# Performance work log

Hardware: AMD Instinct MI355X
Metric: run time of the kernel (lower is better)

## Reference

```python
import jax, jax.numpy as jnp
import numpy as np


def _conv(x, w, padding):
    # x: NCHW, w: OIHW
    return jax.lax.conv_general_dilated(
        x, w, window_strides=(1, 1), padding=padding,
        dimension_numbers=('NCHW', 'OIHW', 'NCHW'))


def setup_inputs() -> dict:
    key = jax.random.key(0)
    ks = jax.random.split(key, 4)
    B, Cin, H, W = 128, 1024, 14, 14
    planes, expansion = 256, 4
    x = jax.random.normal(ks[0], (B, Cin, H, W), dtype=jnp.float32)
    # conv weights (layouts are fully dense since rho=0.0)
    w1 = jax.random.normal(ks[1], (planes, Cin, 1, 1), dtype=jnp.float32) * 0.02
    w2 = jax.random.normal(ks[2], (planes, planes, 3, 3), dtype=jnp.float32) * 0.02
    w3 = jax.random.normal(ks[3], (planes * expansion, planes, 1, 1), dtype=jnp.float32) * 0.02
    # Fixup scalar biases / scale
    z = jnp.zeros((1,), dtype=jnp.float32)
    return {
        'x': x, 'w1': w1, 'w2': w2, 'w3': w3,
        'bias1b': z, 'bias2a': z, 'bias2b': z, 'bias3a': z, 'bias3b': z,
        'rscale': jnp.ones((1,), dtype=jnp.float32), 'rbias': z,
    }


def reference(x, w1, w2, w3, bias1b, bias2a, bias2b, bias3a, bias3b, rscale, rbias):
    # conv1(x) + bias1b  (1x1, fused output bias)
    out = _conv(x, w1, 'VALID') + bias1b[0]
    # conv2(out + bias2a) + bias2b  (3x3, pad 1, fused input+output bias)
    out = _conv(out + bias2a[0], w2, 'SAME') + bias2b[0]
    # conv3(out + bias3a) + bias3b  (1x1)
    out = _conv(out + bias3a[0], w3, 'VALID') + bias3b[0]
    # fused scale + bias + residual ReLU: relu(out*rscale + rbias + identity)
    return jax.nn.relu(out * rscale[0] + rbias[0] + x)
```

## Files before the change

### kernel.cpp

```cpp
#include <hip/hip_runtime.h>
#include <stdint.h>

typedef __bf16 bf16x8 __attribute__((ext_vector_type(8)));
typedef float f32x4 __attribute__((ext_vector_type(4)));
typedef unsigned short u16;

__device__ __forceinline__ u16 f2bf(float f){
  uint32_t u = __float_as_uint(f);
  u = (u + 0x7fffu + ((u >> 16) & 1u)) >> 16;
  return (u16)u;
}
__device__ __forceinline__ float bf2f(u16 v){
  return __uint_as_float(((uint32_t)v) << 16);
}
__device__ __forceinline__ void gl_lds16(const void* g, void* l){
  __builtin_amdgcn_global_load_lds((const __attribute__((address_space(1))) void*)g,
                                   (__attribute__((address_space(3))) void*)l, 16, 0, 0);
}

__global__ __launch_bounds__(256) void prep_w(
    const float* __restrict__ w1, const float* __restrict__ w2,
    const float* __restrict__ w3, u16* __restrict__ wb1, u16* __restrict__ wb2,
    u16* __restrict__ wb3){
  int bid = blockIdx.x, t = threadIdx.x;
  if (bid < 1024){
    int i = bid*256 + t; wb1[i] = f2bf(w1[i]);
  } else if (bid < 3328){
    int i = (bid-1024)*256 + t;
    int o = i / 2304, r = i - o*2304, kq = r >> 8, c = r & 255;
    wb2[i] = f2bf(w2[((size_t)o*256 + c)*9 + kq]);
  } else {
    int i = (bid-3328)*256 + t; wb3[i] = f2bf(w3[i]);
  }
}

__global__ __launch_bounds__(256) void transform_x(const float* __restrict__ x,
                                                   u16* __restrict__ xp0){
  __shared__ float lds[64*201];
  const int b = blockIdx.y, c0 = blockIdx.x*64, t = threadIdx.x;
  const float4* src = (const float4*)x + (size_t)b*50176 + (size_t)c0*49;
  #pragma unroll
  for (int r = 0; r < 13; ++r){
    int q = r*256 + t;
    if (q < 3136){
      unsigned c = (unsigned)q / 49u, f = (unsigned)q - c*49u;
      float4 v = src[q];
      float* d = &lds[c*201 + f*4];
      d[0]=v.x; d[1]=v.y; d[2]=v.z; d[3]=v.w;
    }
  }
  __syncthreads();
  const int c4 = (t & 15)*4, pg = t >> 4;
  #pragma unroll
  for (int r = 0; r < 13; ++r){
    int p = r*16 + pg;
    if (p < 196){
      ushort4 pk;
      ((u16*)&pk)[0] = f2bf(lds[(c4+0)*201 + p]);
      ((u16*)&pk)[1] = f2bf(lds[(c4+1)*201 + p]);
      ((u16*)&pk)[2] = f2bf(lds[(c4+2)*201 + p]);
      ((u16*)&pk)[3] = f2bf(lds[(c4+3)*201 + p]);
      *(ushort4*)&xp0[((size_t)b*196 + p)*1024 + c0 + c4] = pk;
    }
  }
}

__global__ __launch_bounds__(512, 1) void gemm1_conv(
    const u16* __restrict__ A, const u16* __restrict__ B, u16* __restrict__ O,
    const float* __restrict__ s0, const float* __restrict__ s1){
  extern __shared__ char lds[];
  const int t = threadIdx.x, lane = t & 63, w = t >> 6;
  const int wm = (w >> 2) * 64, wn = (w & 3) * 64;
  const int b = blockIdx.x & 127, m0 = (blockIdx.x >> 7) * 128;
  f32x4 acc[4][4] = {};

  uint32_t aoff[2], boff[4];
  #pragma unroll
  for (int i = 0; i < 2; ++i){
    int gl = i*512 + t, row = gl >> 3, ss = gl & 7;
    aoff[i] = (uint32_t)(m0 + row)*2048 + ((ss ^ (row & 7)) << 4);
  }
  #pragma unroll
  for (int i = 0; i < 4; ++i){
    int gl = i*512 + t, row = gl >> 3, ss = gl & 7;
    int y = row >> 4, x = row & 15;
    int p = ((unsigned)(y-1) < 14u && (unsigned)(x-1) < 14u) ? (y-1)*14 + (x-1) : 0;
    boff[i] = ((uint32_t)b*196 + p)*2048 + ((ss ^ (row & 7)) << 4);
  }

  auto stage = [&](int buf, int kc){
    char* Ab = lds + buf*16384;
    char* Bb = lds + 32768 + buf*32768;
    #pragma unroll
    for (int i = 0; i < 2; ++i)
      gl_lds16((const char*)A + aoff[i] + kc*128, Ab + (i*512 + t)*16);
    #pragma unroll
    for (int i = 0; i < 4; ++i)
      gl_lds16((const char*)B + boff[i] + kc*128, Bb + (i*512 + t)*16);
  };
  auto compute = [&](int buf){
    char* Ab = lds + buf*16384;
    char* Bb = lds + 32768 + buf*32768;
    #pragma unroll
    for (int h = 0; h < 2; ++h){
      bf16x8 af[4], bfr[4];
      #pragma unroll
      for (int i = 0; i < 4; ++i){
        int row = wm + i*16 + (lane & 15);
        af[i] = *(const bf16x8*)(Ab + row*128 + (((h*4 + (lane>>4)) ^ (row & 7)) << 4));
      }
      #pragma unroll
      for (int j = 0; j < 4; ++j){
        int row = wn + j*16 + (lane & 15);
        bfr[j] = *(const bf16x8*)(Bb + row*128 + (((h*4 + (lane>>4)) ^ (row & 7)) << 4));
      }
      #pragma unroll
      for (int i = 0; i < 4; ++i)
        #pragma unroll
        for (int j = 0; j < 4; ++j)
          acc[i][j] = __builtin_amdgcn_mfma_f32_16x16x32_bf16(af[i], bfr[j], acc[i][j], 0, 0, 0);
    }
  };

  stage(0, 0);
  __syncthreads();
  #pragma unroll
  for (int kc = 0; kc < 16; ++kc){
    if (kc < 15) stage((kc+1) & 1, kc+1);
    compute(kc & 1);
    __syncthreads();
  }

  float badd = s0[0] + s1[0];
  #pragma unroll
  for (int i = 0; i < 4; ++i){
    int o = m0 + wm + i*16 + ((lane >> 4) << 2);
    #pragma unroll
    for (int j = 0; j < 4; ++j){
      int n = wn + j*16 + (lane & 15);
      int y = n >> 4, x = n & 15;
      bool real = ((unsigned)(y-1) < 14u) && ((unsigned)(x-1) < 14u);
      ushort4 pk;
      #pragma unroll
      for (int q = 0; q < 4; ++q)
        ((u16*)&pk)[q] = real ? f2bf(acc[i][j][q] + badd) : (u16)0;
      *(ushort4*)(O + ((size_t)b*256 + n)*256 + o) = pk;
    }
  }
}

__global__ __launch_bounds__(512, 1) void gemm2_conv(
    const u16* __restrict__ A, const u16* __restrict__ B, u16* __restrict__ O,
    const float* __restrict__ s0, const float* __restrict__ s1){
  extern __shared__ char lds[];
  const int t = threadIdx.x, lane = t & 63, w = t >> 6;
  const int wm = (w >> 2) * 64, wn = (w & 3) * 64;
  const int b = blockIdx.x & 127, m0 = (blockIdx.x >> 7) * 128;
  f32x4 acc[4][4] = {};

  uint32_t aoff[2], boff[5];
  #pragma unroll
  for (int i = 0; i < 2; ++i){
    int gl = i*512 + t, row = gl >> 3, ss = gl & 7;
    aoff[i] = (uint32_t)(m0 + row)*4608 + ((ss ^ (row & 7)) << 4);
  }
  #pragma unroll
  for (int i = 0; i < 5; ++i){
    int gl = i*512 + t, row = gl >> 3, ss = gl & 7;
    int pos = row - 18;
    pos = pos < 0 ? 0 : (pos > 255 ? 255 : pos);
    boff[i] = ((uint32_t)b*256 + pos)*512 + ((ss ^ (row & 7)) << 4);
  }

  auto stageA = [&](int buf, int kq, int kc){
    char* Ab = lds + buf*16384;
    int off = kq*512 + kc*128;
    #pragma unroll
    for (int i = 0; i < 2; ++i)
      gl_lds16((const char*)A + aoff[i] + off, Ab + (i*512 + t)*16);
  };
  auto stageB = [&](int buf, int kc){
    char* Bb = lds + 32768 + buf*37376;
    #pragma unroll
    for (int i = 0; i < 5; ++i){
      int gl = i*512 + t;
      if (gl < 2336) gl_lds16((const char*)B + boff[i] + kc*128, Bb + gl*16);
    }
  };
  auto compute = [&](int ab, int bb, int shift){
    char* Ab = lds + ab*16384;
    char* Bb = lds + 32768 + bb*37376;
    #pragma unroll
    for (int h = 0; h < 2; ++h){
      bf16x8 af[4], bfr[4];
      #pragma unroll
      for (int i = 0; i < 4; ++i){
        int row = wm + i*16 + (lane & 15);
        af[i] = *(const bf16x8*)(Ab + row*128 + (((h*4 + (lane>>4)) ^ (row & 7)) << 4));
      }
      #pragma unroll
      for (int j = 0; j < 4; ++j){
        int row = 18 + wn + j*16 + (lane & 15) + shift;
        bfr[j] = *(const bf16x8*)(Bb + row*128 + (((h*4 + (lane>>4)) ^ (row & 7)) << 4));
      }
      #pragma unroll
      for (int i = 0; i < 4; ++i)
        #pragma unroll
        for (int j = 0; j < 4; ++j)
          acc[i][j] = __builtin_amdgcn_mfma_f32_16x16x32_bf16(af[i], bfr[j], acc[i][j], 0, 0, 0);
    }
  };

  stageB(0, 0); stageA(0, 0, 0);
  __syncthreads();
  int ab = 0, bbuf = 0;
  #pragma unroll
  for (int kc = 0; kc < 4; ++kc){
    #pragma unroll
    for (int kq = 0; kq < 9; ++kq){
      if (kq < 8) stageA(ab ^ 1, kq + 1, kc);
      else if (kc < 3){ stageB(bbuf ^ 1, kc + 1); stageA(ab ^ 1, 0, kc + 1); }
      compute(ab, bbuf, (kq/3 - 1)*16 + (kq%3) - 1);
      __syncthreads();
      ab ^= 1;
      if (kq == 8) bbuf ^= 1;
    }
  }

  float badd = s0[0] + s1[0];
  #pragma unroll
  for (int i = 0; i < 4; ++i){
    int o = m0 + wm + i*16 + ((lane >> 4) << 2);
    #pragma unroll
    for (int j = 0; j < 4; ++j){
      int n = wn + j*16 + (lane & 15);
      int y = n >> 4, x = n & 15;
      if (((unsigned)(y-1) < 14u) && ((unsigned)(x-1) < 14u)){
        int p = (y-1)*14 + (x-1);
        ushort4 pk;
        #pragma unroll
        for (int q = 0; q < 4; ++q) ((u16*)&pk)[q] = f2bf(acc[i][j][q] + badd);
        *(ushort4*)(O + ((size_t)b*196 + p)*256 + o) = pk;
      }
    }
  }
}

__global__ __launch_bounds__(256, 4) void gemm3_conv(
    const u16* __restrict__ A, const u16* __restrict__ B, const u16* __restrict__ xresb,
    float* __restrict__ Of32, const float* __restrict__ s0, const float* __restrict__ s1,
    const float* __restrict__ s2){
  __shared__ char lds[33792];
  const int t = threadIdx.x, lane = t & 63, w = t >> 6;
  const int wm = (w >> 1) * 64, wn = (w & 1) * 64;
  const int orig = blockIdx.x;
  const int bid  = (orig & 7) * ((int)gridDim.x >> 3) + (orig >> 3);
  const int n0 = (bid >> 3) * 128, m0 = (bid & 7) * 128;
  f32x4 acc[4][4] = {};

  uint32_t aoff[4], boff[4];
  #pragma unroll
  for (int i = 0; i < 4; ++i){
    int gl = i*256 + t, row = gl >> 3, ss = gl & 7;
    int xo = (ss ^ (row & 7)) << 4;
    aoff[i] = (uint32_t)(m0 + row)*512 + xo;
    boff[i] = (uint32_t)(n0 + row)*512 + xo;
  }

  auto stage = [&](int s){
    char* Ab = lds;
    char* Bb = lds + 16384;
    #pragma unroll
    for (int i = 0; i < 4; ++i){
      gl_lds16((const char*)A + aoff[i] + s*128, Ab + (i*256 + t)*16);
      gl_lds16((const char*)B + boff[i] + s*128, Bb + (i*256 + t)*16);
    }
  };
  auto compute = [&](){
    char* Ab = lds;
    char* Bb = lds + 16384;
    #pragma unroll
    for (int h = 0; h < 2; ++h){
      bf16x8 af[4], bfr[4];
      #pragma unroll
      for (int i = 0; i < 4; ++i){
        int row = wm + i*16 + (lane & 15);
        af[i] = *(const bf16x8*)(Ab + row*128 + (((h*4 + (lane>>4)) ^ (row & 7)) << 4));
      }
      #pragma unroll
      for (int j = 0; j < 4; ++j){
        int row = wn + j*16 + (lane & 15);
        bfr[j] = *(const bf16x8*)(Bb + row*128 + (((h*4 + (lane>>4)) ^ (row & 7)) << 4));
      }
      #pragma unroll
      for (int i = 0; i < 4; ++i)
        #pragma unroll
        for (int j = 0; j < 4; ++j)
          acc[i][j] = __builtin_amdgcn_mfma_f32_16x16x32_bf16(af[i], bfr[j], acc[i][j], 0, 0, 0);
    }
  };

  #pragma unroll
  for (int s = 0; s < 4; ++s){
    if (s) __syncthreads();
    stage(s);
    __syncthreads();
    compute();
  }

  float b3 = s0[0], rs = s1[0], rbv = s2[0];
  float* ldsF = (float*)lds;
  #pragma unroll
  for (int pass = 0; pass < 2; ++pass){
    __syncthreads();
    if ((wm >> 6) == pass){
      #pragma unroll
      for (int i = 0; i < 4; ++i){
        int rb = i*16 + ((lane >> 4) << 2);
        #pragma unroll
        for (int j = 0; j < 4; ++j){
          int col = wn + j*16 + (lane & 15);
          #pragma unroll
          for (int q = 0; q < 4; ++q) ldsF[(rb + q)*132 + col] = acc[i][j][q];
        }
      }
    }
    __syncthreads();
    #pragma unroll
    for (int r = 0; r < 8; ++r){
      int row = (w << 4) + ((lane >> 5) << 3) + r;
      int n4  = (lane & 31) << 2;
      float4 v = *(float4*)&ldsF[row*132 + n4];
      uint32_t n = n0 + n4;
      uint32_t b = n / 196u, p = n - b*196u;
      int o = m0 + pass*64 + row;
      size_t base = ((size_t)b*1024 + o)*196 + p;
      const u16* xr = xresb + (size_t)n*1024 + o;
      float4 ov;
      ov.x = fmaxf((v.x + b3)*rs + rbv + bf2f(xr[0]),    0.f);
      ov.y = fmaxf((v.y + b3)*rs + rbv + bf2f(xr[1024]), 0.f);
      ov.z = fmaxf((v.z + b3)*rs + rbv + bf2f(xr[2048]), 0.f);
      ov.w = fmaxf((v.w + b3)*rs + rbv + bf2f(xr[3072]), 0.f);
      *(float4*)&Of32[base] = ov;
    }
  }
}

extern "C" void kernel_launch(void* const* d_in, const int* in_sizes, int n_in,
                              void* d_out, int out_size, void* d_ws, size_t ws_size,
                              hipStream_t stream){
  (void)in_sizes; (void)n_in; (void)out_size; (void)ws_size;
  const float* x   = (const float*)d_in[0];
  const float* w1  = (const float*)d_in[1];
  const float* w2  = (const float*)d_in[2];
  const float* w3  = (const float*)d_in[3];
  const float* b1b = (const float*)d_in[4];
  const float* b2a = (const float*)d_in[5];
  const float* b2b = (const float*)d_in[6];
  const float* b3a = (const float*)d_in[7];
  const float* b3b = (const float*)d_in[8];
  const float* rsc = (const float*)d_in[9];
  const float* rbi = (const float*)d_in[10];

  char* ws  = (char*)d_ws;
  u16*  xp1 = (u16*)ws;
  u16*  xp2 = (u16*)(ws + 16777216);
  u16*  xp0 = (u16*)(ws + 29622272);
  u16*  wb1 = (u16*)(ws + 81002496);
  u16*  wb2 = (u16*)(ws + 81526784);
  u16*  wb3 = (u16*)(ws + 82706432);

  prep_w     <<<dim3(4352),   256, 0, stream>>>(w1, w2, w3, wb1, wb2, wb3);
  transform_x<<<dim3(16,128), 256, 0, stream>>>(x, xp0);

  gemm1_conv<<<dim3(256),  512,  98304, stream>>>(wb1, xp0, xp1, b1b, b2a);
  gemm2_conv<<<dim3(256),  512, 107520, stream>>>(wb2, xp1, xp2, b2b, b3a);
  gemm3_conv<<<dim3(1568), 256,      0, stream>>>(wb3, xp2, xp0, (float*)d_out, b3b, rsc, rbi);
}
```

Before: 320.0 us.

## Merge prep kernels, shrink GEMM LDS footprints, read fp32 residual directly

Weight conversion and the x transpose now run in one launch, which removes a kernel launch. gemm1 moves to a smaller K-step with 4-way swizzle and 48KB static LDS, and gemm2 single-buffers the B halo tile to cut LDS from 105KB to 70KB. Both are meant to allow more resident blocks, although 512-thread blocks with 4-per-CU bounds may pressure registers. Block-to-batch mapping changes so the two M halves of a batch are adjacent. The epilogue reads the fp32 residual x directly and coalesced instead of strided bf16, which also fixes a precision loss on the residual. The cost is stalls on gemm2's B reloads, which are no longer overlapped.

```diff
diff --git a/kernel.cpp b/kernel.cpp
--- a/kernel.cpp
+++ b/kernel.cpp
@@ -10,18 +10,17 @@
   u = (u + 0x7fffu + ((u >> 16) & 1u)) >> 16;
   return (u16)u;
 }
-__device__ __forceinline__ float bf2f(u16 v){
-  return __uint_as_float(((uint32_t)v) << 16);
-}
 __device__ __forceinline__ void gl_lds16(const void* g, void* l){
   __builtin_amdgcn_global_load_lds((const __attribute__((address_space(1))) void*)g,
                                    (__attribute__((address_space(3))) void*)l, 16, 0, 0);
 }
 
-__global__ __launch_bounds__(256) void prep_w(
+__global__ __launch_bounds__(256) void prep_transform(
     const float* __restrict__ w1, const float* __restrict__ w2,
-    const float* __restrict__ w3, u16* __restrict__ wb1, u16* __restrict__ wb2,
-    u16* __restrict__ wb3){
+    const float* __restrict__ w3, const float* __restrict__ x,
+    u16* __restrict__ wb1, u16* __restrict__ wb2, u16* __restrict__ wb3,
+    u16* __restrict__ xp0){
+  __shared__ float lds[64*201];
   int bid = blockIdx.x, t = threadIdx.x;
   if (bid < 1024){
     int i = bid*256 + t; wb1[i] = f2bf(w1[i]);
@@ -29,133 +28,121 @@
     int i = (bid-1024)*256 + t;
     int o = i / 2304, r = i - o*2304, kq = r >> 8, c = r & 255;
     wb2[i] = f2bf(w2[((size_t)o*256 + c)*9 + kq]);
+  } else if (bid < 4352){
+    int i = (bid-3328)*256 + t; wb3[i] = f2bf(w3[i]);
   } else {
-    int i = (bid-3328)*256 + t; wb3[i] = f2bf(w3[i]);
-  }
-}
-
-__global__ __launch_bounds__(256) void transform_x(const float* __restrict__ x,
-                                                   u16* __restrict__ xp0){
-  __shared__ float lds[64*201];
-  const int b = blockIdx.y, c0 = blockIdx.x*64, t = threadIdx.x;
-  const float4* src = (const float4*)x + (size_t)b*50176 + (size_t)c0*49;
-  #pragma unroll
-  for (int r = 0; r < 13; ++r){
-    int q = r*256 + t;
-    if (q < 3136){
-      unsigned c = (unsigned)q / 49u, f = (unsigned)q - c*49u;
-      float4 v = src[q];
-      float* d = &lds[c*201 + f*4];
-      d[0]=v.x; d[1]=v.y; d[2]=v.z; d[3]=v.w;
-    }
-  }
+    int lin = bid - 4352;
+    int b = lin >> 4, c0 = (lin & 15)*64;
+    const float4* src = (const float4*)x + (size_t)b*50176 + (size_t)c0*49;
+    #pragma unroll
+    for (int r = 0; r < 13; ++r){
+      int q = r*256 + t;
+      if (q < 3136){
+        unsigned c = (unsigned)q / 49u, f = (unsigned)q - c*49u;
+        float4 v = src[q];
+        float* d = &lds[c*201 + f*4];
+        d[0]=v.x; d[1]=v.y; d[2]=v.z; d[3]=v.w;
+      }
+    }
+    __syncthreads();
+    const int c4 = (t & 15)*4, pg = t >> 4;
+    #pragma unroll
+    for (int r = 0; r < 13; ++r){
+      int p = r*16 + pg;
+      if (p < 196){
+        ushort4 pk;
+        ((u16*)&pk)[0] = f2bf(lds[(c4+0)*201 + p]);
+        ((u16*)&pk)[1] = f2bf(lds[(c4+1)*201 + p]);
+        ((u16*)&pk)[2] = f2bf(lds[(c4+2)*201 + p]);
+        ((u16*)&pk)[3] = f2bf(lds[(c4+3)*201 + p]);
+        *(ushort4*)&xp0[((size_t)b*196 + p)*1024 + c0 + c4] = pk;
+      }
+    }
+  }
+}
+
+__global__ __launch_bounds__(512, 4) void gemm1_conv(
+    const u16* __restrict__ A, const u16* __restrict__ B, u16* __restrict__ O,
+    const float* __restrict__ s0, const float* __restrict__ s1){
+  __shared__ char lds[49152];
+  const int t = threadIdx.x, lane = t & 63, w = t >> 6;
+  const int wm = (w >> 2) * 64, wn = (w & 3) * 64;
+  const int b = blockIdx.x >> 1, m0 = (blockIdx.x & 1) * 128;
+  f32x4 acc[4][4] = {};
+
+  uint32_t aoff, boff[2];
+  { int row = t >> 2, ss = t & 3;
+    aoff = (uint32_t)(m0 + row)*2048 + ((ss ^ (row & 3)) << 4); }
+  #pragma unroll
+  for (int i = 0; i < 2; ++i){
+    int gl = i*512 + t, row = gl >> 2, ss = gl & 3;
+    int y = row >> 4, xx = row & 15;
+    int p = ((unsigned)(y-1) < 14u && (unsigned)(xx-1) < 14u) ? (y-1)*14 + (xx-1) : 0;
+    boff[i] = ((uint32_t)b*196 + p)*2048 + ((ss ^ (row & 3)) << 4);
+  }
+
+  auto stage = [&](int buf, int s){
+    char* Bb = lds + buf*16384;
+    char* Ab = lds + 32768 + buf*8192;
+    gl_lds16((const char*)A + aoff + s*64, Ab + t*16);
+    #pragma unroll
+    for (int i = 0; i < 2; ++i)
+      gl_lds16((const char*)B + boff[i] + s*64, Bb + (i*512 + t)*16);
+  };
+  auto compute = [&](int buf){
+    char* Bb = lds + buf*16384;
+    char* Ab = lds + 32768 + buf*8192;
+    bf16x8 af[4], bfr[4];
+    #pragma unroll
+    for (int i = 0; i < 4; ++i){
+      int row = wm + i*16 + (lane & 15);
+      af[i] = *(const bf16x8*)(Ab + row*64 + (((lane>>4) ^ (row & 3)) << 4));
+    }
+    #pragma unroll
+    for (int j = 0; j < 4; ++j){
+      int row = wn + j*16 + (lane & 15);
+      bfr[j] = *(const bf16x8*)(Bb + row*64 + (((lane>>4) ^ (row & 3)) << 4));
+    }
+    #pragma unroll
+    for (int i = 0; i < 4; ++i)
+      #pragma unroll
+      for (int j = 0; j < 4; ++j)
+        acc[i][j] = __builtin_amdgcn_mfma_f32_16x16x32_bf16(af[i], bfr[j], acc[i][j], 0, 0, 0);
+  };
+
+  stage(0, 0);
   __syncthreads();
-  const int c4 = (t & 15)*4, pg = t >> 4;
-  #pragma unroll
-  for (int r = 0; r < 13; ++r){
-    int p = r*16 + pg;
-    if (p < 196){
+  for (int s = 0; s < 32; ++s){
+    if (s < 31) stage((s+1) & 1, s+1);
+    compute(s & 1);
+    __syncthreads();
+  }
+
+  float badd = s0[0] + s1[0];
+  #pragma unroll
+  for (int i = 0; i < 4; ++i){
+    int o = m0 + wm + i*16 + ((lane >> 4) << 2);
+    #pragma unroll
+    for (int j = 0; j < 4; ++j){
+      int n = wn + j*16 + (lane & 15);
+      int y = n >> 4, xx = n & 15;
+      bool real = ((unsigned)(y-1) < 14u) && ((unsigned)(xx-1) < 14u);
       ushort4 pk;
-      ((u16*)&pk)[0] = f2bf(lds[(c4+0)*201 + p]);
-      ((u16*)&pk)[1] = f2bf(lds[(c4+1)*201 + p]);
-      ((u16*)&pk)[2] = f2bf(lds[(c4+2)*201 + p]);
-      ((u16*)&pk)[3] = f2bf(lds[(c4+3)*201 + p]);
-      *(ushort4*)&xp0[((size_t)b*196 + p)*1024 + c0 + c4] = pk;
-    }
-  }
-}
-
-__global__ __launch_bounds__(512, 1) void gemm1_conv(
+      #pragma unroll
+      for (int q = 0; q < 4; ++q)
+        ((u16*)&pk)[q] = real ? f2bf(acc[i][j][q] + badd) : (u16)0;
+      *(ushort4*)(O + ((size_t)b*256 + n)*256 + o) = pk;
+    }
+  }
+}
+
+__global__ __launch_bounds__(512, 4) void gemm2_conv(
     const u16* __restrict__ A, const u16* __restrict__ B, u16* __restrict__ O,
     const float* __restrict__ s0, const float* __restrict__ s1){
   extern __shared__ char lds[];
   const int t = threadIdx.x, lane = t & 63, w = t >> 6;
   const int wm = (w >> 2) * 64, wn = (w & 3) * 64;
-  const int b = blockIdx.x & 127, m0 = (blockIdx.x >> 7) * 128;
-  f32x4 acc[4][4] = {};
-
-  uint32_t aoff[2], boff[4];
-  #pragma unroll
-  for (int i = 0; i < 2; ++i){
-    int gl = i*512 + t, row = gl >> 3, ss = gl & 7;
-    aoff[i] = (uint32_t)(m0 + row)*2048 + ((ss ^ (row & 7)) << 4);
-  }
-  #pragma unroll
-  for (int i = 0; i < 4; ++i){
-    int gl = i*512 + t, row = gl >> 3, ss = gl & 7;
-    int y = row >> 4, x = row & 15;
-    int p = ((unsigned)(y-1) < 14u && (unsigned)(x-1) < 14u) ? (y-1)*14 + (x-1) : 0;
-    boff[i] = ((uint32_t)b*196 + p)*2048 + ((ss ^ (row & 7)) << 4);
-  }
-
-  auto stage = [&](int buf, int kc){
-    char* Ab = lds + buf*16384;
-    char* Bb = lds + 32768 + buf*32768;
-    #pragma unroll
-    for (int i = 0; i < 2; ++i)
-      gl_lds16((const char*)A + aoff[i] + kc*128, Ab + (i*512 + t)*16);
-    #pragma unroll
-    for (int i = 0; i < 4; ++i)
-      gl_lds16((const char*)B + boff[i] + kc*128, Bb + (i*512 + t)*16);
-  };
-  auto compute = [&](int buf){
-    char* Ab = lds + buf*16384;
-    char* Bb = lds + 32768 + buf*32768;
-    #pragma unroll
-    for (int h = 0; h < 2; ++h){
-      bf16x8 af[4], bfr[4];
-      #pragma unroll
-      for (int i = 0; i < 4; ++i){
-        int row = wm + i*16 + (lane & 15);
-        af[i] = *(const bf16x8*)(Ab + row*128 + (((h*4 + (lane>>4)) ^ (row & 7)) << 4));
-      }
-      #pragma unroll
-      for (int j = 0; j < 4; ++j){
-        int row = wn + j*16 + (lane & 15);
-        bfr[j] = *(const bf16x8*)(Bb + row*128 + (((h*4 + (lane>>4)) ^ (row & 7)) << 4));
-      }
-      #pragma unroll
-      for (int i = 0; i < 4; ++i)
-        #pragma unroll
-        for (int j = 0; j < 4; ++j)
-          acc[i][j] = __builtin_amdgcn_mfma_f32_16x16x32_bf16(af[i], bfr[j], acc[i][j], 0, 0, 0);
-    }
-  };
-
-  stage(0, 0);
-  __syncthreads();
-  #pragma unroll
-  for (int kc = 0; kc < 16; ++kc){
-    if (kc < 15) stage((kc+1) & 1, kc+1);
-    compute(kc & 1);
-    __syncthreads();
-  }
-
-  float badd = s0[0] + s1[0];
-  #pragma unroll
-  for (int i = 0; i < 4; ++i){
-    int o = m0 + wm + i*16 + ((lane >> 4) << 2);
-    #pragma unroll
-    for (int j = 0; j < 4; ++j){
-      int n = wn + j*16 + (lane & 15);
-      int y = n >> 4, x = n & 15;
-      bool real = ((unsigned)(y-1) < 14u) && ((unsigned)(x-1) < 14u);
-      ushort4 pk;
-      #pragma unroll
-      for (int q = 0; q < 4; ++q)
-        ((u16*)&pk)[q] = real ? f2bf(acc[i][j][q] + badd) : (u16)0;
-      *(ushort4*)(O + ((size_t)b*256 + n)*256 + o) = pk;
-    }
-  }
-}
-
-__global__ __launch_bounds__(512, 1) void gemm2_conv(
-    const u16* __restrict__ A, const u16* __restrict__ B, u16* __restrict__ O,
-    const float* __restrict__ s0, const float* __restrict__ s1){
-  extern __shared__ char lds[];
-  const int t = threadIdx.x, lane = t & 63, w = t >> 6;
-  const int wm = (w >> 2) * 64, wn = (w & 3) * 64;
-  const int b = blockIdx.x & 127, m0 = (blockIdx.x >> 7) * 128;
+  const int b = blockIdx.x >> 1, m0 = (blockIdx.x & 1) * 128;
   f32x4 acc[4][4] = {};
 
   uint32_t aoff[2], boff[5];
@@ -179,17 +166,17 @@
     for (int i = 0; i < 2; ++i)
       gl_lds16((const char*)A + aoff[i] + off, Ab + (i*512 + t)*16);
   };
-  auto stageB = [&](int buf, int kc){
-    char* Bb = lds + 32768 + buf*37376;
+  auto stageB = [&](int kc){
+    char* Bb = lds + 32768;
     #pragma unroll
     for (int i = 0; i < 5; ++i){
       int gl = i*512 + t;
       if (gl < 2336) gl_lds16((const char*)B + boff[i] + kc*128, Bb + gl*16);
     }
   };
-  auto compute = [&](int ab, int bb, int shift){
+  auto compute = [&](int ab, int shift){
     char* Ab = lds + ab*16384;
-    char* Bb = lds + 32768 + bb*37376;
+    char* Bb = lds + 32768;
     #pragma unroll
     for (int h = 0; h < 2; ++h){
       bf16x8 af[4], bfr[4];
@@ -211,19 +198,22 @@
     }
   };
 
-  stageB(0, 0); stageA(0, 0, 0);
+  int cur = 0;
+  stageB(0); stageA(cur, 0, 0);
   __syncthreads();
-  int ab = 0, bbuf = 0;
   #pragma unroll
   for (int kc = 0; kc < 4; ++kc){
     #pragma unroll
     for (int kq = 0; kq < 9; ++kq){
-      if (kq < 8) stageA(ab ^ 1, kq + 1, kc);
-      else if (kc < 3){ stageB(bbuf ^ 1, kc + 1); stageA(ab ^ 1, 0, kc + 1); }
-      compute(ab, bbuf, (kq/3 - 1)*16 + (kq%3) - 1);
+      if (kq < 8) stageA(cur ^ 1, kq + 1, kc);
+      compute(cur, (kq/3 - 1)*16 + (kq%3) - 1);
       __syncthreads();
-      ab ^= 1;
-      if (kq == 8) bbuf ^= 1;
+      if (kq < 8) cur ^= 1;
+    }
+    if (kc < 3){
+      stageB(kc + 1); stageA(cur ^ 1, 0, kc + 1);
+      __syncthreads();
+      cur ^= 1;
     }
   }
 
@@ -234,9 +224,9 @@
     #pragma unroll
     for (int j = 0; j < 4; ++j){
       int n = wn + j*16 + (lane & 15);
-      int y = n >> 4, x = n & 15;
-      if (((unsigned)(y-1) < 14u) && ((unsigned)(x-1) < 14u)){
-        int p = (y-1)*14 + (x-1);
+      int y = n >> 4, xx = n & 15;
+      if (((unsigned)(y-1) < 14u) && ((unsigned)(xx-1) < 14u)){
+        int p = (y-1)*14 + (xx-1);
         ushort4 pk;
         #pragma unroll
         for (int q = 0; q < 4; ++q) ((u16*)&pk)[q] = f2bf(acc[i][j][q] + badd);
@@ -247,7 +237,7 @@
 }
 
 __global__ __launch_bounds__(256, 4) void gemm3_conv(
-    const u16* __restrict__ A, const u16* __restrict__ B, const u16* __restrict__ xresb,
+    const u16* __restrict__ A, const u16* __restrict__ B, const float* __restrict__ xres,
     float* __restrict__ Of32, const float* __restrict__ s0, const float* __restrict__ s1,
     const float* __restrict__ s2){
   __shared__ char lds[33792];
@@ -335,12 +325,12 @@
       uint32_t b = n / 196u, p = n - b*196u;
       int o = m0 + pass*64 + row;
       size_t base = ((size_t)b*1024 + o)*196 + p;
-      const u16* xr = xresb + (size_t)n*1024 + o;
+      float4 xr = *(const float4*)&xres[base];
       float4 ov;
-      ov.x = fmaxf((v.x + b3)*rs + rbv + bf2f(xr[0]),    0.f);
-      ov.y = fmaxf((v.y + b3)*rs + rbv + bf2f(xr[1024]), 0.f);
-      ov.z = fmaxf((v.z + b3)*rs + rbv + bf2f(xr[2048]), 0.f);
-      ov.w = fmaxf((v.w + b3)*rs + rbv + bf2f(xr[3072]), 0.f);
+      ov.x = fmaxf((v.x + b3)*rs + rbv + xr.x, 0.f);
+      ov.y = fmaxf((v.y + b3)*rs + rbv + xr.y, 0.f);
+      ov.z = fmaxf((v.z + b3)*rs + rbv + xr.z, 0.f);
+      ov.w = fmaxf((v.w + b3)*rs + rbv + xr.w, 0.f);
       *(float4*)&Of32[base] = ov;
     }
   }
@@ -370,10 +360,9 @@
   u16*  wb2 = (u16*)(ws + 81526784);
   u16*  wb3 = (u16*)(ws + 82706432);
 
-  prep_w     <<<dim3(4352),   256, 0, stream>>>(w1, w2, w3, wb1, wb2, wb3);
-  transform_x<<<dim3(16,128), 256, 0, stream>>>(x, xp0);
-
-  gemm1_conv<<<dim3(256),  512,  98304, stream>>>(wb1, xp0, xp1, b1b, b2a);
-  gemm2_conv<<<dim3(256),  512, 107520, stream>>>(wb2, xp1, xp2, b2b, b3a);
-  gemm3_conv<<<dim3(1568), 256,      0, stream>>>(wb3, xp2, xp0, (float*)d_out, b3b, rsc, rbi);
-}
+  prep_transform<<<dim3(6400), 256, 0, stream>>>(w1, w2, w3, x, wb1, wb2, wb3, xp0);
+
+  gemm1_conv<<<dim3(256),  512,     0, stream>>>(wb1, xp0, xp1, b1b, b2a);
+  gemm2_conv<<<dim3(256),  512, 70144, stream>>>(wb2, xp1, xp2, b2b, b3a);
+  gemm3_conv<<<dim3(1568), 256,     0, stream>>>(wb3, xp2, x, (float*)d_out, b3b, rsc, rbi);
+}
```

New measurement: 324.1 us. No clear change (+1.3%).
